# Optimization experiments

Hardware: AMD Instinct MI355X
Metric: run time of the kernel (lower is better)

Reference implementation:

```python
import jax, jax.numpy as jnp
import numpy as np

N_NODES = 100000
N_EDGES = 6400000
HID = 32


def setup_inputs() -> dict:
    key = jax.random.key(0)
    ks = jax.random.split(key, 24)
    inp = {
        "x_G": jax.random.normal(ks[0], (N_NODES, 1), dtype=jnp.float32),
        "edge_index_G": jax.random.randint(ks[1], (2, N_EDGES), 0, N_NODES, dtype=jnp.int32),
        "x_H": jax.random.normal(ks[2], (N_NODES, 1), dtype=jnp.float32),
        "edge_index_H": jax.random.randint(ks[3], (2, N_EDGES), 0, N_NODES, dtype=jnp.int32),
    }
    ki = 4
    for i in range(3):
        d_in = 1 if i == 0 else HID
        inp[f"W1_{i}"] = jax.random.normal(ks[ki], (d_in, HID), dtype=jnp.float32) / np.sqrt(d_in); ki += 1
        inp[f"b1_{i}"] = jnp.zeros((HID,), dtype=jnp.float32)
        inp[f"W2_{i}"] = jax.random.normal(ks[ki], (HID, HID), dtype=jnp.float32) / np.sqrt(HID); ki += 1
        inp[f"b2_{i}"] = jnp.zeros((HID,), dtype=jnp.float32)
    inp["Wc1"] = jax.random.normal(ks[ki], (2 * HID, HID), dtype=jnp.float32) / np.sqrt(2 * HID); ki += 1
    inp["bc1"] = jnp.zeros((HID,), dtype=jnp.float32)
    inp["Wc2"] = jax.random.normal(ks[ki], (HID, 1), dtype=jnp.float32) / np.sqrt(HID); ki += 1
    inp["bc2"] = jnp.zeros((1,), dtype=jnp.float32)
    return inp


def _encode(x, edge_index, layers):
    n = x.shape[0]
    src, dst = edge_index[0], edge_index[1]
    for (W1, b1, W2, b2) in layers:
        # GIN aggregation: sum of neighbor messages scattered to targets; eps = 0
        agg = jax.ops.segment_sum(x[src], dst, num_segments=n)  # [N, d]
        h = x + agg  # (1 + eps) * x + agg with eps = 0
        h = jax.nn.relu(h @ W1 + b1) @ W2 + b2  # GIN MLP
        x = jax.nn.relu(h)  # outer F.relu in encode loop
    return jnp.sum(x, axis=0, keepdims=True)  # global_add_pool, single graph -> [1, HID]


def reference(x_G, edge_index_G, x_H, edge_index_H,
              W1_0, b1_0, W2_0, b2_0,
              W1_1, b1_1, W2_1, b2_1,
              W1_2, b1_2, W2_2, b2_2,
              Wc1, bc1, Wc2, bc2):
    layers = [(W1_0, b1_0, W2_0, b2_0),
              (W1_1, b1_1, W2_1, b2_1),
              (W1_2, b1_2, W2_2, b2_2)]
    h_G = _encode(x_G, edge_index_G, layers)
    h_H = _encode(x_H, edge_index_H, layers)
    combined = jnp.concatenate([h_G, h_H], axis=1)  # [1, 2*HID]
    out = jax.nn.relu(combined @ Wc1 + bc1) @ Wc2 + bc2
    return jax.nn.sigmoid(out)
```

## Files before the change

kernel.cpp:

```cpp
#include <hip/hip_runtime.h>
#include <hip/hip_bf16.h>
#include <math.h>
#include <string.h>

#define HID 32
#define PSHIFT 8
#define NPB (1 << PSHIFT)
#define MAXP 512
#define SLOTS 17408
#define GS 32
#define HS_ROWS 32
#define COLBUF 3072
#define COLBUF0 6144
typedef unsigned short u16;
typedef unsigned char u8;
typedef float f32x2 __attribute__((ext_vector_type(2)));

__device__ inline float e42f_sw(unsigned b) {
    unsigned u = (b & 0x7fu) << 20;
    float f; memcpy(&f, &u, 4);
    return f * 0x1p120f;
}
__device__ inline unsigned f2e4_sw(float f) {
    f = fminf(f, 448.f);
    float y = f * 0x1p-120f;
    unsigned r; memcpy(&r, &y, 4);
    r = r + 0x7FFFFu + ((r >> 20) & 1u);
    return (r >> 20) & 0x7fu;
}
__device__ inline void acc_e4(float* a, unsigned w) {
#if __has_builtin(__builtin_amdgcn_cvt_pk_f32_fp8)
    f32x2 lo = __builtin_amdgcn_cvt_pk_f32_fp8(w, false);
    f32x2 hi = __builtin_amdgcn_cvt_pk_f32_fp8(w, true);
    a[0] += lo.x; a[1] += lo.y; a[2] += hi.x; a[3] += hi.y;
#else
    a[0] += e42f_sw(w);
    a[1] += e42f_sw(w >> 8);
    a[2] += e42f_sw(w >> 16);
    a[3] += e42f_sw(w >> 24);
#endif
}
__device__ inline unsigned pack_e4(float o0, float o1, float o2, float o3) {
#if __has_builtin(__builtin_amdgcn_cvt_pk_fp8_f32)
    unsigned pw = (unsigned)__builtin_amdgcn_cvt_pk_fp8_f32(
        fminf(o0, 448.f), fminf(o1, 448.f), 0, false);
    pw = (unsigned)__builtin_amdgcn_cvt_pk_fp8_f32(
        fminf(o2, 448.f), fminf(o3, 448.f), pw, true);
    return pw;
#else
    return f2e4_sw(o0) | (f2e4_sw(o1) << 8) | (f2e4_sw(o2) << 16) | (f2e4_sw(o3) << 24);
#endif
}

__global__ void zero_kernel(float* __restrict__ p, int n) {
    int i = blockIdx.x * blockDim.x + threadIdx.x;
    if (i < n) p[i] = 0.f;
}
__global__ void init_gcur2(int* __restrict__ gA, int* __restrict__ gB, int P) {
    int i = blockIdx.x * blockDim.x + threadIdx.x;
    if (i < P) gA[i * GS] = i * SLOTS;
    else if (i < 2 * P) { int b = i - P; gB[b * GS] = b * SLOTS; }
}

__global__ void partition_edges(const int* __restrict__ srcA, const int* __restrict__ dstA,
                                int* __restrict__ gcurA, unsigned* __restrict__ stagedA,
                                const int* __restrict__ srcB, const int* __restrict__ dstB,
                                int* __restrict__ gcurB, unsigned* __restrict__ stagedB,
                                int gsplit, int E, int P) {
    __shared__ int h[4][MAXP];
    __shared__ int hbase[MAXP];
    __shared__ int cur[MAXP];
    __shared__ int gbase[MAXP];
    __shared__ unsigned sortedv[4096];
    __shared__ u16 bktid[4096];
    __shared__ int wsums[4];
    __shared__ int sTotal;
    const int* src; const int* dst; int* gcur; unsigned* staged;
    int bid = blockIdx.x;
    if (bid < gsplit) { src = srcA; dst = dstA; gcur = gcurA; staged = stagedA; }
    else { bid -= gsplit; src = srcB; dst = dstB; gcur = gcurB; staged = stagedB; }

    int t = threadIdx.x, wid = t >> 6, lane = t & 63;
    for (int i = t; i < 4 * MAXP; i += 256) (&h[0][0])[i] = 0;
    __syncthreads();

    int base = bid * 4096;
    int4 S[4], D[4];
#pragma unroll
    for (int r = 0; r < 4; r++) {
        int e = base + r * 1024 + t * 4;
        if (e + 3 < E) {
            S[r] = *(const int4*)(src + e);
            D[r] = *(const int4*)(dst + e);
        } else {
            int s0[4], d0[4];
            for (int j = 0; j < 4; j++) {
                int ee = e + j;
                s0[j] = (ee < E) ? src[ee] : -1;
                d0[j] = (ee < E) ? dst[ee] : -1;
            }
            S[r] = make_int4(s0[0], s0[1], s0[2], s0[3]);
            D[r] = make_int4(d0[0], d0[1], d0[2], d0[3]);
        }
        if (D[r].x >= 0) atomicAdd(&h[wid][D[r].x >> PSHIFT], 1);
        if (D[r].y >= 0) atomicAdd(&h[wid][D[r].y >> PSHIFT], 1);
        if (D[r].z >= 0) atomicAdd(&h[wid][D[r].z >> PSHIFT], 1);
        if (D[r].w >= 0) atomicAdd(&h[wid][D[r].w >> PSHIFT], 1);
    }
    __syncthreads();

    int b0 = 2 * t, b1 = 2 * t + 1;
    int t0 = (b0 < P) ? (h[0][b0] + h[1][b0] + h[2][b0] + h[3][b0]) : 0;
    int t1 = (b1 < P) ? (h[0][b1] + h[1][b1] + h[2][b1] + h[3][b1]) : 0;
    int s = t0 + t1;
    int incl = s;
#pragma unroll
    for (int off = 1; off < 64; off <<= 1) {
        int u = __shfl_up(incl, off, 64);
        if (lane >= off) incl += u;
    }
    if (lane == 63) wsums[wid] = incl;
    __syncthreads();
    int woff = 0;
#pragma unroll
    for (int w = 0; w < 4; w++) if (w < wid) woff += wsums[w];
    int excl = woff + incl - s;
    if (b0 < P) { hbase[b0] = excl;      cur[b0] = excl; }
    if (b1 < P) { hbase[b1] = excl + t0; cur[b1] = excl + t0; }
    if (b0 < P && t0) gbase[b0] = atomicAdd(&gcur[b0 * GS], t0);
    if (b1 < P && t1) gbase[b1] = atomicAdd(&gcur[b1 * GS], t1);
    if (t == 255) sTotal = excl + s;
    __syncthreads();

#pragma unroll
    for (int r = 0; r < 4; r++) {
        int ss[4] = { S[r].x, S[r].y, S[r].z, S[r].w };
        int dd[4] = { D[r].x, D[r].y, D[r].z, D[r].w };
#pragma unroll
        for (int j = 0; j < 4; j++) {
            int d = dd[j];
            if (d >= 0) {
                int bk = d >> PSHIFT;
                int pos = atomicAdd(&cur[bk], 1);
                sortedv[pos] = ((unsigned)(d & (NPB - 1)) << 17) | (unsigned)ss[j];
                bktid[pos]   = (u16)bk;
            }
        }
    }
    __syncthreads();

    int total = sTotal;
    for (int i = t; i < total; i += 256) {
        int bk = bktid[i];
        int addr = gbase[bk] + (i - hbase[bk]);
        if (addr < (bk + 1) * SLOTS)
            staged[addr] = sortedv[i];
    }
}

__global__ void scan_buckets(const int* __restrict__ gcurA, int* __restrict__ colbaseA,
                             int* __restrict__ rowptrA,
                             const int* __restrict__ gcurB, int* __restrict__ colbaseB,
                             int* __restrict__ rowptrB, int P, int N) {
    __shared__ int wsums[4];
    const int* gcur; int* colbase; int* rowptr;
    if (blockIdx.x == 0) { gcur = gcurA; colbase = colbaseA; rowptr = rowptrA; }
    else { gcur = gcurB; colbase = colbaseB; rowptr = rowptrB; }
    int t = threadIdx.x, wid = t >> 6, lane = t & 63;
    int b0 = 2 * t, b1 = 2 * t + 1;
    int c0 = 0, c1 = 0;
    if (b0 < P) { c0 = gcur[b0 * GS] - b0 * SLOTS; if (c0 > SLOTS) c0 = SLOTS; }
    if (b1 < P) { c1 = gcur[b1 * GS] - b1 * SLOTS; if (c1 > SLOTS) c1 = SLOTS; }
    int s = c0 + c1;
    int incl = s;
#pragma unroll
    for (int off = 1; off < 64; off <<= 1) {
        int u = __shfl_up(incl, off, 64);
        if (lane >= off) incl += u;
    }
    if (lane == 63) wsums[wid] = incl;
    __syncthreads();
    int woff = 0;
#pragma unroll
    for (int w = 0; w < 4; w++) if (w < wid) woff += wsums[w];
    int excl = woff + incl - s;
    if (b0 < P) colbase[b0] = excl;
    if (b1 < P) colbase[b1] = excl + c0;
    if (t == 255) {
        colbase[P] = excl + s;
        rowptr[N]  = excl + s;
    }
}

__global__ void sort_bucket(const unsigned* __restrict__ stagedA, const int* __restrict__ gcurA,
                            const int* __restrict__ colbaseA, int* __restrict__ rowptrA,
                            int* __restrict__ colA,
                            const unsigned* __restrict__ stagedB, const int* __restrict__ gcurB,
                            const int* __restrict__ colbaseB, int* __restrict__ rowptrB,
                            int* __restrict__ colB,
                            int gsplit, int N) {
    __shared__ int cnt[NPB];
    __shared__ int wsum[4];
    __shared__ int sorted[SLOTS];
    const unsigned* staged; const int* gcur; const int* colbase; int* rowptr; int* col;
    int b = blockIdx.x;
    if (b < gsplit) { staged = stagedA; gcur = gcurA; colbase = colbaseA; rowptr = rowptrA; col = colA; }
    else { b -= gsplit; staged = stagedB; gcur = gcurB; colbase = colbaseB; rowptr = rowptrB; col = colB; }
    int t = threadIdx.x, lane = t & 63, wid = t >> 6;
    int sBeg = b * SLOTS;
    int sEnd = gcur[b * GS]; if (sEnd > sBeg + SLOTS) sEnd = sBeg + SLOTS;
    int total = sEnd - sBeg;
    int colStart = colbase[b];
    int nodeBase = b << PSHIFT;

    cnt[t] = 0;
    __syncthreads();
    for (int i = sBeg + t; i < sEnd; i += 256)
        atomicAdd(&cnt[staged[i] >> 17], 1);
    __syncthreads();

    int myc = cnt[t];
    int incl = myc;
#pragma unroll
    for (int off = 1; off < 64; off <<= 1) {
        int u = __shfl_up(incl, off, 64);
        if (lane >= off) incl += u;
    }
    if (lane == 63) wsum[wid] = incl;
    __syncthreads();
    int woff = 0;
#pragma unroll
    for (int w = 0; w < 4; w++) if (w < wid) woff += wsum[w];
    int excl = woff + incl - myc;
    int node = nodeBase + t;
    if (node < N) rowptr[node] = colStart + excl;
    __syncthreads();
    cnt[t] = excl;
    __syncthreads();

    for (int i = sBeg + t; i < sEnd; i += 256) {
        unsigned w = staged[i];
        int pos = atomicAdd(&cnt[w >> 17], 1);
        sorted[pos] = (int)(w & 0x1FFFFu);
    }
    __syncthreads();
    for (int i = t; i < total; i += 256)
        col[colStart + i] = sorted[i];
}

__global__ void mlp0_fused(const int* __restrict__ rowptrA, const int* __restrict__ colA,
                           const float* __restrict__ x0A, u8* __restrict__ outA,
                           const int* __restrict__ rowptrB, const int* __restrict__ colB,
                           const float* __restrict__ x0B, u8* __restrict__ outB,
                           const float* __restrict__ W1, const float* __restrict__ b1,
                           const float* __restrict__ W2, const float* __restrict__ b2,
                           int gsplit, int n) {
    __shared__ float sW1[HID], sb1[HID], sW2[HID * HID], sb2[HID];
    __shared__ int colbuf[COLBUF0];
    const int* rowptr; const int* col; const float* x0; u8* out;
    int bid = blockIdx.x;
    if (bid < gsplit) { rowptr = rowptrA; col = colA; x0 = x0A; out = outA; }
    else { bid -= gsplit; rowptr = rowptrB; col = colB; x0 = x0B; out = outB; }
    int t = threadIdx.x;
    if (t < HID) { sW1[t] = W1[t]; sb1[t] = b1[t]; sb2[t] = b2[t]; }
    for (int i = t; i < HID * HID; i += blockDim.x) sW2[i] = W2[i];

    int firstNode = bid * 64;
    int lastNode  = firstNode + 64; if (lastNode > n) lastNode = n;
    int blockStart = (firstNode < n) ? rowptr[firstNode] : 0;
    int blockEnd   = (firstNode < n) ? rowptr[lastNode] : 0;
    int stagedCnt = blockEnd - blockStart; if (stagedCnt > COLBUF0) stagedCnt = COLBUF0;
    for (int i = t; i < stagedCnt; i += 256) colbuf[i] = col[blockStart + i];
    __syncthreads();

    int node = firstNode + (t >> 2);
    int q    = t & 3;
    int lane = t & 63;
    int base = lane & ~3;
    bool active = node < n;

    float s = 0.f;
    if (active) {
        int beg = rowptr[node], end = rowptr[node + 1];
        int jSplit = blockStart + stagedCnt; if (jSplit > end) jSplit = end;
        int j = beg + q;
        for (; j + 12 < jSplit; j += 16) {
            int c0 = colbuf[j - blockStart];
            int c1 = colbuf[j + 4 - blockStart];
            int c2 = colbuf[j + 8 - blockStart];
            int c3 = colbuf[j + 12 - blockStart];
            s += x0[c0]; s += x0[c1]; s += x0[c2]; s += x0[c3];
        }
        for (; j < jSplit; j += 4) s += x0[colbuf[j - blockStart]];
        for (; j < end; j += 4) s += x0[col[j]];
    }
    s += __shfl_xor(s, 1, 64);
    s += __shfl_xor(s, 2, 64);
    float v = active ? (x0[node] + s) : 0.f;

    float h[8];
#pragma unroll
    for (int i = 0; i < 8; i++) h[i] = fmaxf(fmaf(v, sW1[q * 8 + i], sb1[q * 8 + i]), 0.f);
    float o[8];
#pragma unroll
    for (int i = 0; i < 8; i++) o[i] = sb2[q * 8 + i];
#pragma unroll
    for (int k = 0; k < HID; k++) {
        float hk = __shfl(h[k & 7], base | (k >> 3), 64);
#pragma unroll
        for (int i = 0; i < 8; i++) o[i] = fmaf(hk, sW2[k * HID + q * 8 + i], o[i]);
    }
    if (active) {
        unsigned w0 = pack_e4(fmaxf(o[0], 0.f), fmaxf(o[1], 0.f),
                              fmaxf(o[2], 0.f), fmaxf(o[3], 0.f));
        unsigned w1 = pack_e4(fmaxf(o[4], 0.f), fmaxf(o[5], 0.f),
                              fmaxf(o[6], 0.f), fmaxf(o[7], 0.f));
        uint2 pk = make_uint2(w0, w1);
        *(uint2*)(out + ((size_t)node << 5) + (q << 3)) = pk;
    }
}

template <bool REDUCE>
__global__ void mlp_fused(const int* __restrict__ rowptrA, const int* __restrict__ colA,
                          const u8* __restrict__ xinA, u8* __restrict__ xoutA,
                          float* __restrict__ hsumA,
                          const int* __restrict__ rowptrB, const int* __restrict__ colB,
                          const u8* __restrict__ xinB, u8* __restrict__ xoutB,
                          float* __restrict__ hsumB,
                          const float* __restrict__ W1, const float* __restrict__ b1,
                          const float* __restrict__ W2, const float* __restrict__ b2,
                          int gsplit, int n) {
    __shared__ float sW1[HID * HID], sb1[HID], sW2[HID * HID], sb2[HID];
    __shared__ int colbuf[COLBUF];
    __shared__ float red[4][HID];
    const int* rowptr; const int* col; const u8* xin; u8* xout; float* hsum;
    int bid = blockIdx.x;
    if (bid < gsplit) { rowptr = rowptrA; col = colA; xin = xinA; xout = xoutA; hsum = hsumA; }
    else { bid -= gsplit; rowptr = rowptrB; col = colB; xin = xinB; xout = xoutB; hsum = hsumB; }
    int t = threadIdx.x;
    for (int i = t; i < HID * HID; i += blockDim.x) { sW1[i] = W1[i]; sW2[i] = W2[i]; }
    if (t < HID) { sb1[t] = b1[t]; sb2[t] = b2[t]; }

    int firstNode = bid * 32;
    int lastNode  = firstNode + 32; if (lastNode > n) lastNode = n;
    int blockStart = (firstNode < n) ? rowptr[firstNode] : 0;
    int blockEnd   = (firstNode < n) ? rowptr[lastNode] : 0;
    int stagedCnt = blockEnd - blockStart; if (stagedCnt > COLBUF) stagedCnt = COLBUF;
    for (int i = t; i < stagedCnt; i += 256) colbuf[i] = col[blockStart + i];
    __syncthreads();

    int node = firstNode + (t >> 3);
    int q    = t & 7;
    int lane = t & 63;
    int base = lane & ~7;
    bool active = node < n;

    float va[4];
#pragma unroll
    for (int i = 0; i < 4; i++) va[i] = 0.f;
    if (active) {
        int beg = rowptr[node], end = rowptr[node + 1];
        const u8* xq = xin + (q << 2);
        float a0[4], a1[4], a2[4], a3[4];
#pragma unroll
        for (int i = 0; i < 4; i++) a0[i] = a1[i] = a2[i] = a3[i] = 0.f;
        {
            unsigned w = *(const unsigned*)(xq + ((size_t)node << 5));
            acc_e4(a0, w);
        }
        int jSplit = blockStart + stagedCnt; if (jSplit > end) jSplit = end;
        int j = beg;
        for (; j + 8 <= jSplit; j += 8) {
            int lj = j - blockStart;
            int c0 = colbuf[lj+0], c1 = colbuf[lj+1], c2 = colbuf[lj+2], c3 = colbuf[lj+3];
            int c4 = colbuf[lj+4], c5 = colbuf[lj+5], c6 = colbuf[lj+6], c7 = colbuf[lj+7];
            unsigned w0 = *(const unsigned*)(xq + ((size_t)c0 << 5));
            unsigned w1 = *(const unsigned*)(xq + ((size_t)c1 << 5));
            unsigned w2 = *(const unsigned*)(xq + ((size_t)c2 << 5));
            unsigned w3 = *(const unsigned*)(xq + ((size_t)c3 << 5));
            unsigned w4 = *(const unsigned*)(xq + ((size_t)c4 << 5));
            unsigned w5 = *(const unsigned*)(xq + ((size_t)c5 << 5));
            unsigned w6 = *(const unsigned*)(xq + ((size_t)c6 << 5));
            unsigned w7 = *(const unsigned*)(xq + ((size_t)c7 << 5));
            acc_e4(a0, w0); acc_e4(a1, w1); acc_e4(a2, w2); acc_e4(a3, w3);
            acc_e4(a0, w4); acc_e4(a1, w5); acc_e4(a2, w6); acc_e4(a3, w7);
        }
        for (; j < jSplit; j++) {
            unsigned w = *(const unsigned*)(xq + ((size_t)colbuf[j - blockStart] << 5));
            acc_e4(a0, w);
        }
        for (; j < end; j++) {
            unsigned w = *(const unsigned*)(xq + ((size_t)col[j] << 5));
            acc_e4(a0, w);
        }
#pragma unroll
        for (int i = 0; i < 4; i++) va[i] = (a0[i] + a1[i]) + (a2[i] + a3[i]);
    }

    float h[4];
#pragma unroll
    for (int i = 0; i < 4; i++) h[i] = sb1[q * 4 + i];
#pragma unroll
    for (int k = 0; k < HID; k++) {
        float vk = __shfl(va[k & 3], base | (k >> 2), 64);
#pragma unroll
        for (int i = 0; i < 4; i++) h[i] = fmaf(vk, sW1[k * HID + q * 4 + i], h[i]);
    }
#pragma unroll
    for (int i = 0; i < 4; i++) h[i] = fmaxf(h[i], 0.f);

    float o[4];
#pragma unroll
    for (int i = 0; i < 4; i++) o[i] = sb2[q * 4 + i];
#pragma unroll
    for (int k = 0; k < HID; k++) {
        float hk = __shfl(h[k & 3], base | (k >> 2), 64);
#pragma unroll
        for (int i = 0; i < 4; i++) o[i] = fmaf(hk, sW2[k * HID + q * 4 + i], o[i]);
    }
#pragma unroll
    for (int i = 0; i < 4; i++) o[i] = fmaxf(o[i], 0.f);

    if (REDUCE) {
        if (!active) {
#pragma unroll
            for (int i = 0; i < 4; i++) o[i] = 0.f;
        }
#pragma unroll
        for (int i = 0; i < 4; i++) {
            float v = o[i];
            v += __shfl_xor(v, 8, 64);
            v += __shfl_xor(v, 16, 64);
            v += __shfl_xor(v, 32, 64);
            o[i] = v;
        }
        int wid = t >> 6;
        if (lane < 8) {
#pragma unroll
            for (int i = 0; i < 4; i++) red[wid][lane * 4 + i] = o[i];
        }
        __syncthreads();
        if (t < HID) {
            float s = red[0][t] + red[1][t] + red[2][t] + red[3][t];
            atomicAdd(&hsum[(blockIdx.x & (HS_ROWS - 1)) * (2 * HID) + t], s);
        }
    } else if (active) {
        unsigned pw = pack_e4(o[0], o[1], o[2], o[3]);
        *(unsigned*)(xout + ((size_t)node << 5) + (q << 2)) = pw;
    }
}

__global__ void head_kernel(const float* __restrict__ hsumP,
                            const float* __restrict__ Wc1, const float* __restrict__ bc1,
                            const float* __restrict__ Wc2, const float* __restrict__ bc2,
                            float* __restrict__ out) {
    __shared__ float hs[2 * HID];
    int t = threadIdx.x;
    if (t < 2 * HID) {
        float s = 0.f;
        for (int r = 0; r < HS_ROWS; r++) s += hsumP[r * (2 * HID) + t];
        hs[t] = s;
    }
    __syncthreads();
    float val = 0.f;
    if (t < HID) {
        float acc = bc1[t];
        for (int i = 0; i < 2 * HID; i++) acc = fmaf(hs[i], Wc1[i * HID + t], acc);
        val = fmaxf(acc, 0.f) * Wc2[t];
    }
    for (int off = 32; off >= 1; off >>= 1) val += __shfl_xor(val, off, 64);
    if (t == 0) out[0] = 1.f / (1.f + expf(-(val + bc2[0])));
}

extern "C" void kernel_launch(void* const* d_in, const int* in_sizes, int n_in,
                              void* d_out, int out_size, void* d_ws, size_t ws_size,
                              hipStream_t stream) {
    const float* xg[2] = { (const float*)d_in[0], (const float*)d_in[2] };
    const int*   eg[2] = { (const int*)d_in[1],   (const int*)d_in[3] };
    const float* W1[3] = { (const float*)d_in[4], (const float*)d_in[8],  (const float*)d_in[12] };
    const float* b1[3] = { (const float*)d_in[5], (const float*)d_in[9],  (const float*)d_in[13] };
    const float* W2[3] = { (const float*)d_in[6], (const float*)d_in[10], (const float*)d_in[14] };
    const float* b2[3] = { (const float*)d_in[7], (const float*)d_in[11], (const float*)d_in[15] };
    const float* Wc1 = (const float*)d_in[16];
    const float* bc1 = (const float*)d_in[17];
    const float* Wc2 = (const float*)d_in[18];
    const float* bc2 = (const float*)d_in[19];

    const int N = in_sizes[0];
    const int E = in_sizes[1] / 2;
    const int P = (N + NPB - 1) >> PSHIFT;

    const int TB = 256;
    dim3 blk(TB);
    int gE4k = (E + 4095) / 4096;
    int gN64 = (N + 63) / 64;
    int gN8  = (N + 31) / 32;

    size_t szB    = (size_t)N * 32;
    size_t szRow  = (size_t)(N + 1) * 4;
    size_t szCol  = (size_t)E * 4;
    size_t szCb   = (size_t)(P + 1) * 4;
    size_t szGcur = (size_t)P * GS * 4;
    size_t szStg  = (size_t)P * SLOTS * 4;
    size_t szHsum = (size_t)HS_ROWS * 2 * HID * 4;
    size_t needBatched = 4 * szB + szHsum + 2 * (szRow + szCol + szCb + szGcur + szStg) + 4096;

    char* w = (char*)d_ws;
    auto take = [&](size_t sz) { char* p = w; w += (sz + 255) & ~(size_t)255; return p; };

    if (ws_size >= needBatched) {
        u8*    B0[2]  = { (u8*)take(szB), (u8*)take(szB) };
        u8*    B1[2]  = { (u8*)take(szB), (u8*)take(szB) };
        float* hsumP  = (float*)take(szHsum);
        int*   rowp[2] = { (int*)take(szRow), (int*)take(szRow) };
        int*   col[2]  = { (int*)take(szCol), (int*)take(szCol) };
        int*   cb[2]   = { (int*)take(szCb), (int*)take(szCb) };
        int*   gc[2]   = { (int*)take(szGcur), (int*)take(szGcur) };
        unsigned* st[2] = { (unsigned*)take(szStg), (unsigned*)take(szStg) };

        zero_kernel<<<(HS_ROWS * 2 * HID + 255) / 256, 256, 0, stream>>>(hsumP, HS_ROWS * 2 * HID);
        init_gcur2<<<(2 * P + TB - 1) / TB, blk, 0, stream>>>(gc[0], gc[1], P);
        partition_edges<<<2 * gE4k, blk, 0, stream>>>(eg[0], eg[0] + E, gc[0], st[0],
                                                      eg[1], eg[1] + E, gc[1], st[1],
                                                      gE4k, E, P);
        scan_buckets<<<2, blk, 0, stream>>>(gc[0], cb[0], rowp[0], gc[1], cb[1], rowp[1], P, N);
        sort_bucket<<<2 * P, blk, 0, stream>>>(st[0], gc[0], cb[0], rowp[0], col[0],
                                               st[1], gc[1], cb[1], rowp[1], col[1], P, N);
        mlp0_fused<<<2 * gN64, blk, 0, stream>>>(rowp[0], col[0], xg[0], B0[0],
                                                 rowp[1], col[1], xg[1], B0[1],
                                                 W1[0], b1[0], W2[0], b2[0], gN64, N);
        mlp_fused<false><<<2 * gN8, blk, 0, stream>>>(rowp[0], col[0], B0[0], B1[0], nullptr,
                                                      rowp[1], col[1], B0[1], B1[1], nullptr,
                                                      W1[1], b1[1], W2[1], b2[1], gN8, N);
        mlp_fused<true><<<2 * gN8, blk, 0, stream>>>(rowp[0], col[0], B1[0], nullptr, hsumP,
                                                     rowp[1], col[1], B1[1], nullptr, hsumP + HID,
                                                     W1[2], b1[2], W2[2], b2[2], gN8, N);
        head_kernel<<<1, 64, 0, stream>>>(hsumP, Wc1, bc1, Wc2, bc2, (float*)d_out);
    } else {
        u8*    B0s    = (u8*)take(szB);
        u8*    B1s    = (u8*)take(szB);
        float* hsumP  = (float*)take(szHsum);
        int*   rowp   = (int*)take(szRow);
        int*   colp   = (int*)take(szCol);
        int*   cbp    = (int*)take(szCb);
        int*   gcp    = (int*)take(szGcur);
        unsigned* stp = (unsigned*)take(szStg);

        zero_kernel<<<(HS_ROWS * 2 * HID + 255) / 256, 256, 0, stream>>>(hsumP, HS_ROWS * 2 * HID);
        for (int g = 0; g < 2; g++) {
            const float* x0  = xg[g];
            const int*   src = eg[g];
            const int*   dst = src + E;
            init_gcur2<<<(P + TB - 1) / TB, blk, 0, stream>>>(gcp, gcp, P);
            partition_edges<<<gE4k, blk, 0, stream>>>(src, dst, gcp, stp,
                                                      src, dst, gcp, stp, gE4k, E, P);
            scan_buckets<<<1, blk, 0, stream>>>(gcp, cbp, rowp, gcp, cbp, rowp, P, N);
            sort_bucket<<<P, blk, 0, stream>>>(stp, gcp, cbp, rowp, colp,
                                               stp, gcp, cbp, rowp, colp, P, N);
            mlp0_fused<<<gN64, blk, 0, stream>>>(rowp, colp, x0, B0s,
                                                 rowp, colp, x0, B0s,
                                                 W1[0], b1[0], W2[0], b2[0], gN64, N);
            mlp_fused<false><<<gN8, blk, 0, stream>>>(rowp, colp, B0s, B1s, nullptr,
                                                      rowp, colp, B0s, B1s, nullptr,
                                                      W1[1], b1[1], W2[1], b2[1], gN8, N);
            mlp_fused<true><<<gN8, blk, 0, stream>>>(rowp, colp, B1s, nullptr, hsumP + g * HID,
                                                     rowp, colp, B1s, nullptr, hsumP + g * HID,
                                                     W1[2], b1[2], W2[2], b2[2], gN8, N);
        }
        head_kernel<<<1, 64, 0, stream>>>(hsumP, Wc1, bc1, Wc2, bc2, (float*)d_out);
    }
}
```

Measured before the change: 526.8 us.

## Scatter partitioned edges directly to global using histogram-atomic ranks

The partition kernel now keeps the return value of the per-wave histogram atomic as each edge's rank within its bucket and turns the histogram into per-wave offsets. Each edge is then written straight to its global staged slot, with no block-wide scan, no LDS sort buffer and no second copy pass. This cuts shared memory use (more blocks can fit per CU), removes a barrier and the second atomic pass, but the global writes are less coalesced because they are no longer contiguous per bucket.

```diff
diff --git a/kernel.cpp b/kernel.cpp
--- a/kernel.cpp
+++ b/kernel.cpp
@@ -68,13 +68,8 @@
                                 int* __restrict__ gcurB, unsigned* __restrict__ stagedB,
                                 int gsplit, int E, int P) {
     __shared__ int h[4][MAXP];
-    __shared__ int hbase[MAXP];
-    __shared__ int cur[MAXP];
     __shared__ int gbase[MAXP];
-    __shared__ unsigned sortedv[4096];
-    __shared__ u16 bktid[4096];
     __shared__ int wsums[4];
-    __shared__ int sTotal;
     const int* src; const int* dst; int* gcur; unsigned* staged;
     int bid = blockIdx.x;
     if (bid < gsplit) { src = srcA; dst = dstA; gcur = gcurA; staged = stagedA; }
@@ -86,6 +81,7 @@
 
     int base = bid * 4096;
     int4 S[4], D[4];
+    u16 pos[16];
 #pragma unroll
     for (int r = 0; r < 4; r++) {
         int e = base + r * 1024 + t * 4;
@@ -102,34 +98,26 @@
             S[r] = make_int4(s0[0], s0[1], s0[2], s0[3]);
             D[r] = make_int4(d0[0], d0[1], d0[2], d0[3]);
         }
-        if (D[r].x >= 0) atomicAdd(&h[wid][D[r].x >> PSHIFT], 1);
-        if (D[r].y >= 0) atomicAdd(&h[wid][D[r].y >> PSHIFT], 1);
-        if (D[r].z >= 0) atomicAdd(&h[wid][D[r].z >> PSHIFT], 1);
-        if (D[r].w >= 0) atomicAdd(&h[wid][D[r].w >> PSHIFT], 1);
+        if (D[r].x >= 0) pos[r*4+0] = (u16)atomicAdd(&h[wid][D[r].x >> PSHIFT], 1);
+        if (D[r].y >= 0) pos[r*4+1] = (u16)atomicAdd(&h[wid][D[r].y >> PSHIFT], 1);
+        if (D[r].z >= 0) pos[r*4+2] = (u16)atomicAdd(&h[wid][D[r].z >> PSHIFT], 1);
+        if (D[r].w >= 0) pos[r*4+3] = (u16)atomicAdd(&h[wid][D[r].w >> PSHIFT], 1);
     }
     __syncthreads();
 
     int b0 = 2 * t, b1 = 2 * t + 1;
-    int t0 = (b0 < P) ? (h[0][b0] + h[1][b0] + h[2][b0] + h[3][b0]) : 0;
-    int t1 = (b1 < P) ? (h[0][b1] + h[1][b1] + h[2][b1] + h[3][b1]) : 0;
-    int s = t0 + t1;
-    int incl = s;
-#pragma unroll
-    for (int off = 1; off < 64; off <<= 1) {
-        int u = __shfl_up(incl, off, 64);
-        if (lane >= off) incl += u;
-    }
-    if (lane == 63) wsums[wid] = incl;
-    __syncthreads();
-    int woff = 0;
-#pragma unroll
-    for (int w = 0; w < 4; w++) if (w < wid) woff += wsums[w];
-    int excl = woff + incl - s;
-    if (b0 < P) { hbase[b0] = excl;      cur[b0] = excl; }
-    if (b1 < P) { hbase[b1] = excl + t0; cur[b1] = excl + t0; }
-    if (b0 < P && t0) gbase[b0] = atomicAdd(&gcur[b0 * GS], t0);
-    if (b1 < P && t1) gbase[b1] = atomicAdd(&gcur[b1 * GS], t1);
-    if (t == 255) sTotal = excl + s;
+    if (b0 < P) {
+        int c0 = h[0][b0], c1 = h[1][b0], c2 = h[2][b0], c3 = h[3][b0];
+        int tot = c0 + c1 + c2 + c3;
+        if (tot) gbase[b0] = atomicAdd(&gcur[b0 * GS], tot);
+        h[0][b0] = 0; h[1][b0] = c0; h[2][b0] = c0 + c1; h[3][b0] = c0 + c1 + c2;
+    }
+    if (b1 < P) {
+        int c0 = h[0][b1], c1 = h[1][b1], c2 = h[2][b1], c3 = h[3][b1];
+        int tot = c0 + c1 + c2 + c3;
+        if (tot) gbase[b1] = atomicAdd(&gcur[b1 * GS], tot);
+        h[0][b1] = 0; h[1][b1] = c0; h[2][b1] = c0 + c1; h[3][b1] = c0 + c1 + c2;
+    }
     __syncthreads();
 
 #pragma unroll
@@ -141,20 +129,11 @@
             int d = dd[j];
             if (d >= 0) {
                 int bk = d >> PSHIFT;
-                int pos = atomicAdd(&cur[bk], 1);
-                sortedv[pos] = ((unsigned)(d & (NPB - 1)) << 17) | (unsigned)ss[j];
-                bktid[pos]   = (u16)bk;
+                int addr = gbase[bk] + h[wid][bk] + (int)pos[r*4+j];
+                if (addr < (bk + 1) * SLOTS)
+                    staged[addr] = ((unsigned)(d & (NPB - 1)) << 17) | (unsigned)ss[j];
             }
         }
-    }
-    __syncthreads();
-
-    int total = sTotal;
-    for (int i = t; i < total; i += 256) {
-        int bk = bktid[i];
-        int addr = gbase[bk] + (i - hbase[bk]);
-        if (addr < (bk + 1) * SLOTS)
-            staged[addr] = sortedv[i];
     }
 }
 
```

Result: slower. 552.1 us (+4.8%).
